# Kernel optimization log

Hardware: AMD Instinct MI355X
Metric: run time of the kernel (lower is better)

Reference implementation:

```python
import jax, jax.numpy as jnp
import numpy as np

def setup_inputs() -> dict:
    key = jax.random.key(0)
    k1, k2, k3, k4, k5 = jax.random.split(key, 5)
    H = 1024
    B, T = 32, 1024
    hidden = jax.random.normal(k1, (1, B, H), dtype=jnp.float32)
    encoder_outputs = jax.random.normal(k2, (B, T, H), dtype=jnp.float32)
    # nn.Linear(2H, H): weight [H, 2H], bias [H]
    bound = 1.0 / np.sqrt(2 * H)
    W = jax.random.uniform(k3, (H, 2 * H), minval=-bound, maxval=bound, dtype=jnp.float32)
    b = jax.random.uniform(k4, (H,), minval=-bound, maxval=bound, dtype=jnp.float32)
    v = jax.random.uniform(k5, (H,), dtype=jnp.float32)  # torch.rand
    return {"hidden": hidden, "encoder_outputs": encoder_outputs, "W": W, "b": b, "v": v}

def reference(hidden, encoder_outputs, W, b, v):
    B = hidden.shape[1]
    H = hidden.shape[2]
    h = jnp.transpose(hidden, (1, 0, 2)).reshape(B, -1)  # [B, H]
    # Split Linear(2H->H): cat([h_rep, enc]) @ W.T == h @ Wh.T + enc @ We.T
    Wh, We = W[:, :H], W[:, H:]
    # [B,1,H] + [B,T,H] -> [B,T,H]
    pre = jnp.tanh((h @ Wh.T + b)[:, None, :] + jnp.einsum('bth,gh->btg', encoder_outputs, We))
    energies = jnp.einsum('bth,h->bt', pre, v)  # [B, T]
    return jax.nn.softmax(energies, axis=1)[:, None, :]  # [B, 1, T]
```

## Files before the change

### kernel.cpp

```cpp
#include <hip/hip_runtime.h>
#include <hip/hip_fp16.h>

typedef _Float16 half8   __attribute__((ext_vector_type(8)));
typedef _Float16 half4_t __attribute__((ext_vector_type(4)));
typedef float    f32x4   __attribute__((ext_vector_type(4)));

#define HDIM  1024
#define BATCH 32
#define TLEN  1024
#define M_TOT (BATCH * TLEN)

#define BM 128
#define BN 128
#define BKF 64
#define LDA 40

__global__ void prep_k(const float* __restrict__ W, const float* __restrict__ hidden,
                       const float* __restrict__ bias, _Float16* __restrict__ We16,
                       float* __restrict__ q, float* __restrict__ energ) {
    const int bid = blockIdx.x;
    const int t = threadIdx.x;
    if (bid < 1024) {
        int idx = bid * 256 + t;
        int g  = idx >> 8;
        int k4 = idx & 255;
        float4 f = *reinterpret_cast<const float4*>(W + (size_t)g * 2048 + 1024 + k4 * 4);
        half4_t h;
        h[0] = (_Float16)f.x; h[1] = (_Float16)f.y; h[2] = (_Float16)f.z; h[3] = (_Float16)f.w;
        *reinterpret_cast<half4_t*>(We16 + (size_t)idx * 4) = h;
    } else if (bid < 2048) {
        int g = bid - 1024;
        int wave = t >> 6, lane = t & 63;
        float acc[BATCH];
#pragma unroll
        for (int b = 0; b < BATCH; b++) acc[b] = 0.f;
        const float* wr = W + (size_t)g * 2048;
        for (int h = t; h < HDIM; h += 256) {
            float w = wr[h];
#pragma unroll
            for (int b = 0; b < BATCH; b++) acc[b] = fmaf(w, hidden[b * HDIM + h], acc[b]);
        }
        __shared__ float sm[4 * BATCH];
#pragma unroll
        for (int b = 0; b < BATCH; b++) {
            float s = acc[b];
#pragma unroll
            for (int off = 32; off >= 1; off >>= 1) s += __shfl_xor(s, off);
            if (lane == 0) sm[wave * BATCH + b] = s;
        }
        __syncthreads();
        if (t < BATCH) {
            float s = sm[t] + sm[BATCH + t] + sm[2 * BATCH + t] + sm[3 * BATCH + t];
            q[t * HDIM + g] = s + bias[g];
        }
    } else {
        energ[(bid - 2048) * 256 + t] = 0.f;
    }
}

__global__ void enc_convert_k(const float* __restrict__ enc, _Float16* __restrict__ enc16) {
    size_t i = ((size_t)blockIdx.x * blockDim.x + threadIdx.x) * 8;
    float4 f0 = *reinterpret_cast<const float4*>(enc + i);
    float4 f1 = *reinterpret_cast<const float4*>(enc + i + 4);
    half8 h;
    h[0] = (_Float16)f0.x; h[1] = (_Float16)f0.y; h[2] = (_Float16)f0.z; h[3] = (_Float16)f0.w;
    h[4] = (_Float16)f1.x; h[5] = (_Float16)f1.y; h[6] = (_Float16)f1.z; h[7] = (_Float16)f1.w;
    *reinterpret_cast<half8*>(enc16 + i) = h;
}

__device__ __forceinline__ void async16(const void* g, void* l) {
    __builtin_amdgcn_global_load_lds(
        (const __attribute__((address_space(1))) void*)g,
        (__attribute__((address_space(3))) void*)l, 16, 0, 0);
}

__global__ __launch_bounds__(256)
void attn_gemm_lds_k(const _Float16* __restrict__ enc16,
                     const _Float16* __restrict__ We16,
                     const float* __restrict__ q, const float* __restrict__ v,
                     float* __restrict__ energies) {
    __shared__ _Float16 As[BM * BKF];
    __shared__ _Float16 Bs[BN * BKF];

    const int tid  = threadIdx.x;
    const int id   = blockIdx.x;
    const int xcd  = id & 7;
    const int w    = id >> 3;
    const int m0   = (xcd * 32 + (w >> 3)) * BM;
    const int n0   = (w & 7) * BN;
    const int wave = tid >> 6;
    const int lane = tid & 63;
    const int quad = lane >> 4;
    const int l16  = lane & 15;
    const int wm   = (wave & 1) * 64;
    const int wn   = (wave >> 1) * 64;

    f32x4 acc[4][4];
#pragma unroll
    for (int i = 0; i < 4; i++)
#pragma unroll
        for (int j = 0; j < 4; j++) acc[i][j] = {0.f, 0.f, 0.f, 0.f};

    const int srow = wave * 32 + (lane >> 3);
    const int scol = ((lane & 7) ^ (lane >> 3)) * 8;
    const _Float16* gA = enc16 + (size_t)(m0 + srow) * HDIM + scol;
    const _Float16* gB = We16  + (size_t)(n0 + srow) * HDIM + scol;
    _Float16* lA = As + wave * 2048;
    _Float16* lB = Bs + wave * 2048;
    const size_t istep = (size_t)8 * HDIM;

#pragma unroll
    for (int ii = 0; ii < 4; ii++) {
        async16(gA + ii * istep, lA + ii * 512);
        async16(gB + ii * istep, lB + ii * 512);
    }
    __syncthreads();

    int aoff[2][4], boff[2][4];
#pragma unroll
    for (int s = 0; s < 2; s++)
#pragma unroll
        for (int i = 0; i < 4; i++) {
            int ra = wm + i * 16 + l16;
            int rb = wn + i * 16 + l16;
            aoff[s][i] = ra * BKF + (((s * 4 + quad) ^ (l16 & 7)) * 8);
            boff[s][i] = rb * BKF + (((s * 4 + quad) ^ (l16 & 7)) * 8);
        }

    for (int k0 = 0; k0 < HDIM; k0 += BKF) {
        half8 af[2][4], bf[2][4];
#pragma unroll
        for (int s = 0; s < 2; s++)
#pragma unroll
            for (int i = 0; i < 4; i++) {
                af[s][i] = *reinterpret_cast<const half8*>(&As[aoff[s][i]]);
                bf[s][i] = *reinterpret_cast<const half8*>(&Bs[boff[s][i]]);
            }
        __syncthreads();

        if (k0 + BKF < HDIM) {
            const int kn = k0 + BKF;
#pragma unroll
            for (int ii = 0; ii < 4; ii++) {
                async16(gA + kn + ii * istep, lA + ii * 512);
                async16(gB + kn + ii * istep, lB + ii * 512);
            }
        }

#pragma unroll
        for (int s = 0; s < 2; s++)
#pragma unroll
            for (int mi = 0; mi < 4; mi++)
#pragma unroll
                for (int ni = 0; ni < 4; ni++)
                    acc[mi][ni] = __builtin_amdgcn_mfma_f32_16x16x32_f16(af[s][mi], bf[s][ni], acc[mi][ni], 0, 0, 0);

        __syncthreads();
    }

    const int bidx = m0 >> 10;
    float qv[4], vv[4];
#pragma unroll
    for (int ni = 0; ni < 4; ni++) {
        int g = n0 + wn + ni * 16 + l16;
        qv[ni] = q[bidx * HDIM + g];
        vv[ni] = v[g];
    }
#pragma unroll
    for (int mi = 0; mi < 4; mi++) {
#pragma unroll
        for (int r = 0; r < 4; r++) {
            int row = wm + mi * 16 + quad * 4 + r;
            float s = 0.f;
#pragma unroll
            for (int ni = 0; ni < 4; ni++) {
                float pre = acc[mi][ni][r] + qv[ni];
                float e = __expf(2.f * pre);
                float th = 1.f - 2.f / (e + 1.f);
                s = fmaf(th, vv[ni], s);
            }
            s += __shfl_xor(s, 1);
            s += __shfl_xor(s, 2);
            s += __shfl_xor(s, 4);
            s += __shfl_xor(s, 8);
            if (l16 == 0) atomicAdd(&energies[m0 + row], s);
        }
    }
}

__global__ __launch_bounds__(256, 2)
void attn_gemm_k(const float* __restrict__ enc, const _Float16* __restrict__ We16,
                 const float* __restrict__ q, const float* __restrict__ v,
                 float* __restrict__ energies) {
    __shared__ _Float16 As[BM * LDA];
    __shared__ _Float16 Bs[BN * LDA];

    const int tid  = threadIdx.x;
    const int m0   = blockIdx.x * BM;
    const int n0   = blockIdx.y * BN;
    const int wave = tid >> 6;
    const int lane = tid & 63;
    const int quad = lane >> 4;
    const int l16  = lane & 15;
    const int wm   = (wave & 1) * 64;
    const int wn   = (wave >> 1) * 64;

    const int srow = tid >> 1;
    const int scol = (tid & 1) * 16;

    f32x4 acc[4][4];
#pragma unroll
    for (int i = 0; i < 4; i++)
#pragma unroll
        for (int j = 0; j < 4; j++) acc[i][j] = {0.f, 0.f, 0.f, 0.f};

    const float*    ag = enc  + (size_t)(m0 + srow) * HDIM + scol;
    const _Float16* bg = We16 + (size_t)(n0 + srow) * HDIM + scol;
    _Float16* aw = &As[srow * LDA + scol];
    _Float16* bw = &Bs[srow * LDA + scol];

    for (int k0 = 0; k0 < HDIM; k0 += 32) {
        float4 a0 = *reinterpret_cast<const float4*>(ag + k0 + 0);
        float4 a1 = *reinterpret_cast<const float4*>(ag + k0 + 4);
        float4 a2 = *reinterpret_cast<const float4*>(ag + k0 + 8);
        float4 a3 = *reinterpret_cast<const float4*>(ag + k0 + 12);
        float4 b0 = *reinterpret_cast<const float4*>(bg + k0);
        float4 b1 = *reinterpret_cast<const float4*>(bg + k0 + 8);

        __syncthreads();

        half8 ha0, ha1;
        ha0[0] = (_Float16)a0.x; ha0[1] = (_Float16)a0.y; ha0[2] = (_Float16)a0.z; ha0[3] = (_Float16)a0.w;
        ha0[4] = (_Float16)a1.x; ha0[5] = (_Float16)a1.y; ha0[6] = (_Float16)a1.z; ha0[7] = (_Float16)a1.w;
        ha1[0] = (_Float16)a2.x; ha1[1] = (_Float16)a2.y; ha1[2] = (_Float16)a2.z; ha1[3] = (_Float16)a2.w;
        ha1[4] = (_Float16)a3.x; ha1[5] = (_Float16)a3.y; ha1[6] = (_Float16)a3.z; ha1[7] = (_Float16)a3.w;
        *reinterpret_cast<half8*>(aw)     = ha0;
        *reinterpret_cast<half8*>(aw + 8) = ha1;
        *reinterpret_cast<float4*>(bw)     = b0;
        *reinterpret_cast<float4*>(bw + 8) = b1;

        __syncthreads();

        half8 af[4], bf[4];
#pragma unroll
        for (int i = 0; i < 4; i++) {
            af[i] = *reinterpret_cast<const half8*>(&As[(wm + i * 16 + l16) * LDA + quad * 8]);
            bf[i] = *reinterpret_cast<const half8*>(&Bs[(wn + i * 16 + l16) * LDA + quad * 8]);
        }
#pragma unroll
        for (int mi = 0; mi < 4; mi++)
#pragma unroll
            for (int ni = 0; ni < 4; ni++)
                acc[mi][ni] = __builtin_amdgcn_mfma_f32_16x16x32_f16(af[mi], bf[ni], acc[mi][ni], 0, 0, 0);
    }

    const int bidx = m0 >> 10;
    float qv[4], vv[4];
#pragma unroll
    for (int ni = 0; ni < 4; ni++) {
        int g = n0 + wn + ni * 16 + l16;
        qv[ni] = q[bidx * HDIM + g];
        vv[ni] = v[g];
    }
#pragma unroll
    for (int mi = 0; mi < 4; mi++) {
#pragma unroll
        for (int r = 0; r < 4; r++) {
            int row = wm + mi * 16 + quad * 4 + r;
            float s = 0.f;
#pragma unroll
            for (int ni = 0; ni < 4; ni++) {
                float pre = acc[mi][ni][r] + qv[ni];
                float e = __expf(2.f * pre);
                float th = 1.f - 2.f / (e + 1.f);
                s = fmaf(th, vv[ni], s);
            }
            s += __shfl_xor(s, 1);
            s += __shfl_xor(s, 2);
            s += __shfl_xor(s, 4);
            s += __shfl_xor(s, 8);
            if (l16 == 0) atomicAdd(&energies[m0 + row], s);
        }
    }
}

__global__ void softmax_k(const float* __restrict__ energies, float* __restrict__ out) {
    int b = blockIdx.x;
    int t = threadIdx.x;
    int wave = t >> 6, lane = t & 63;
    __shared__ float smax[4], ssum[4];
    float e[4];
#pragma unroll
    for (int i = 0; i < 4; i++) e[i] = energies[b * TLEN + t + i * 256];
    float m = fmaxf(fmaxf(e[0], e[1]), fmaxf(e[2], e[3]));
#pragma unroll
    for (int off = 32; off >= 1; off >>= 1) m = fmaxf(m, __shfl_xor(m, off));
    if (lane == 0) smax[wave] = m;
    __syncthreads();
    float M = fmaxf(fmaxf(smax[0], smax[1]), fmaxf(smax[2], smax[3]));
    float x[4]; float s = 0.f;
#pragma unroll
    for (int i = 0; i < 4; i++) { x[i] = __expf(e[i] - M); s += x[i]; }
#pragma unroll
    for (int off = 32; off >= 1; off >>= 1) s += __shfl_xor(s, off);
    if (lane == 0) ssum[wave] = s;
    __syncthreads();
    float S = ssum[0] + ssum[1] + ssum[2] + ssum[3];
    float inv = 1.f / S;
#pragma unroll
    for (int i = 0; i < 4; i++) out[b * TLEN + t + i * 256] = x[i] * inv;
}

extern "C" void kernel_launch(void* const* d_in, const int* in_sizes, int n_in,
                              void* d_out, int out_size, void* d_ws, size_t ws_size,
                              hipStream_t stream) {
    const float* hidden = (const float*)d_in[0];
    const float* enc    = (const float*)d_in[1];
    const float* W      = (const float*)d_in[2];
    const float* bias   = (const float*)d_in[3];
    const float* v      = (const float*)d_in[4];
    float* out = (float*)d_out;

    char* ws = (char*)d_ws;
    float*    q     = (float*)ws;
    float*    energ = (float*)(ws + 131072);
    _Float16* We16  = (_Float16*)(ws + 262144);
    _Float16* enc16 = (_Float16*)(ws + 262144 + 2097152);
    const size_t need_fast = 262144 + 2097152 + (size_t)M_TOT * HDIM * 2;

    prep_k<<<dim3(2176), 256, 0, stream>>>(W, hidden, bias, We16, q, energ);
    if (ws_size >= need_fast) {
        enc_convert_k<<<dim3((size_t)M_TOT * HDIM / 8 / 256), 256, 0, stream>>>(enc, enc16);
        attn_gemm_lds_k<<<dim3(2048), 256, 0, stream>>>(enc16, We16, q, v, energ);
    } else {
        attn_gemm_k<<<dim3(256, 8), 256, 0, stream>>>(enc, We16, q, v, energ);
    }
    softmax_k<<<dim3(BATCH), 256, 0, stream>>>(energ, out);
}
```

Measured before the change: 309.5 us.

## Replace LDS GEMM with 256x256-tile 8-wave double-buffered ping-pong kernel

Swaps the 128x128 single-buffer fp16 GEMM for a 256x256-tile, 512-thread kernel. It double-buffers LDS with direct global-to-LDS loads and interleaves staged fragment reads, MFMA sub-blocks and barriers with setprio hints. The goal is more reuse per loaded byte and hiding global load latency behind MFMA work. In exchange it uses 128KB of LDS per block and many more accumulator registers, and it relies on hand-tuned waitcnt counts for correctness.

```diff
diff --git a/kernel.cpp b/kernel.cpp
--- a/kernel.cpp
+++ b/kernel.cpp
@@ -12,7 +12,6 @@
 
 #define BM 128
 #define BN 128
-#define BKF 64
 #define LDA 40
 
 __global__ void prep_k(const float* __restrict__ W, const float* __restrict__ hidden,
@@ -74,20 +73,169 @@
         (__attribute__((address_space(3))) void*)l, 16, 0, 0);
 }
 
-__global__ __launch_bounds__(256)
-void attn_gemm_lds_k(const _Float16* __restrict__ enc16,
-                     const _Float16* __restrict__ We16,
-                     const float* __restrict__ q, const float* __restrict__ v,
-                     float* __restrict__ energies) {
-    __shared__ _Float16 As[BM * BKF];
-    __shared__ _Float16 Bs[BN * BKF];
+#define NIT 8
+
+__global__ __launch_bounds__(512, 2)
+void attn_gemm8_k(const _Float16* __restrict__ enc16,
+                  const _Float16* __restrict__ We16,
+                  const float* __restrict__ q, const float* __restrict__ v,
+                  float* __restrict__ energies) {
+    __shared__ _Float16 lds[65536];
 
     const int tid  = threadIdx.x;
     const int id   = blockIdx.x;
     const int xcd  = id & 7;
     const int w    = id >> 3;
-    const int m0   = (xcd * 32 + (w >> 3)) * BM;
-    const int n0   = (w & 7) * BN;
+    const int m0   = (xcd * 16 + (w >> 2)) * 256;
+    const int n0   = (w & 3) * 256;
+
+    const int wave = tid >> 6;
+    const int lane = tid & 63;
+    const int quad = lane >> 4;
+    const int l16  = lane & 15;
+    const int wm   = wave >> 2;
+    const int wn   = wave & 3;
+    const int hb   = wn >> 1;
+
+    const int rA = tid >> 3;
+    const int sc = ((tid & 7) ^ (rA & 7)) * 8;
+    const _Float16* gA = enc16 + (size_t)(m0 + rA) * HDIM + sc;
+    const _Float16* gB = We16  + (size_t)(n0 + rA) * HDIM + sc;
+
+    const int cs0 = (quad ^ (l16 & 7)) * 8;
+    const int cs1 = ((4 + quad) ^ (l16 & 7)) * 8;
+    const int arow = wm * 8192 + l16 * 64;
+    const int brow = 16384 + hb * 8192 + ((wn & 1) * 64 + l16) * 64;
+
+    f32x4 acc[8][4];
+#pragma unroll
+    for (int i = 0; i < 8; i++)
+#pragma unroll
+        for (int j = 0; j < 4; j++) acc[i][j] = {0.f, 0.f, 0.f, 0.f};
+
+    half8 aLo[4][2], aHi[4][2], bLo[2][2], bHi[2][2];
+
+#define STAGE_A(buf, ha, kt) do { \
+    _Float16* d_ = &lds[(buf)*32768 + (ha)*8192 + tid*8]; \
+    const _Float16* s_ = gA + (size_t)(ha)*131072 + (kt)*64; \
+    async16(s_, d_); async16(s_ + 65536, d_ + 4096); } while(0)
+
+#define STAGE_B(buf, hbt, kt) do { \
+    _Float16* d_ = &lds[(buf)*32768 + 16384 + (hbt)*8192 + tid*8]; \
+    const _Float16* s_ = gB + (size_t)(hbt)*131072 + (kt)*64; \
+    async16(s_, d_); async16(s_ + 65536, d_ + 4096); } while(0)
+
+#define RD_ALO(bb) { _Pragma("unroll") for (int mi_ = 0; mi_ < 4; mi_++) { \
+    aLo[mi_][0] = *reinterpret_cast<const half8*>(&lds[(bb)+arow+mi_*1024+cs0]); \
+    aLo[mi_][1] = *reinterpret_cast<const half8*>(&lds[(bb)+arow+mi_*1024+cs1]); } }
+#define RD_AHI(bb) { _Pragma("unroll") for (int mi_ = 0; mi_ < 4; mi_++) { \
+    aHi[mi_][0] = *reinterpret_cast<const half8*>(&lds[(bb)+arow+(mi_+4)*1024+cs0]); \
+    aHi[mi_][1] = *reinterpret_cast<const half8*>(&lds[(bb)+arow+(mi_+4)*1024+cs1]); } }
+#define RD_BLO(bb) { _Pragma("unroll") for (int ni_ = 0; ni_ < 2; ni_++) { \
+    bLo[ni_][0] = *reinterpret_cast<const half8*>(&lds[(bb)+brow+ni_*1024+cs0]); \
+    bLo[ni_][1] = *reinterpret_cast<const half8*>(&lds[(bb)+brow+ni_*1024+cs1]); } }
+#define RD_BHI(bb) { _Pragma("unroll") for (int ni_ = 0; ni_ < 2; ni_++) { \
+    bHi[ni_][0] = *reinterpret_cast<const half8*>(&lds[(bb)+brow+(ni_+2)*1024+cs0]); \
+    bHi[ni_][1] = *reinterpret_cast<const half8*>(&lds[(bb)+brow+(ni_+2)*1024+cs1]); } }
+
+#define MFMA16(AF, BF, MO, NO) { _Pragma("unroll") for (int ks_ = 0; ks_ < 2; ks_++) \
+    _Pragma("unroll") for (int mi_ = 0; mi_ < 4; mi_++) \
+    _Pragma("unroll") for (int ni_ = 0; ni_ < 2; ni_++) \
+      acc[mi_+MO][ni_+NO] = __builtin_amdgcn_mfma_f32_16x16x32_f16( \
+          AF[mi_][ks_], BF[ni_][ks_], acc[mi_+MO][ni_+NO], 0, 0, 0); }
+
+#define BAR1 { __builtin_amdgcn_s_barrier(); \
+    asm volatile("s_waitcnt lgkmcnt(0)" ::: "memory"); \
+    __builtin_amdgcn_sched_barrier(0); \
+    __builtin_amdgcn_s_setprio(1); }
+#define BAR2 { __builtin_amdgcn_s_setprio(0); \
+    __builtin_amdgcn_s_barrier(); \
+    __builtin_amdgcn_sched_barrier(0); }
+#define BAR2V(n) { __builtin_amdgcn_s_setprio(0); \
+    asm volatile("s_waitcnt vmcnt(" #n ")" ::: "memory"); \
+    __builtin_amdgcn_s_barrier(); \
+    __builtin_amdgcn_sched_barrier(0); }
+
+    STAGE_A(0, 0, 0); STAGE_A(0, 1, 0); STAGE_B(0, 0, 0); STAGE_B(0, 1, 0);
+    STAGE_B(1, 0, 1); STAGE_B(1, 1, 1);
+    asm volatile("s_waitcnt vmcnt(4)" ::: "memory");
+    __builtin_amdgcn_s_barrier();
+    __builtin_amdgcn_sched_barrier(0);
+
+    for (int i = 0; i < NIT; i++) {
+        const int kt1 = 2 * i + 1, kt2 = 2 * i + 2, kt3 = 2 * i + 3;
+        const bool more = (i < NIT - 1);
+        RD_ALO(0); RD_BLO(0);            STAGE_A(1, 0, kt1);
+        BAR1; MFMA16(aLo, bLo, 0, 0); BAR2;
+        RD_BHI(0);                       STAGE_A(1, 1, kt1);
+        BAR1; MFMA16(aLo, bHi, 0, 2); BAR2;
+        RD_AHI(0);                       if (more) STAGE_B(0, 0, kt2);
+        BAR1; MFMA16(aHi, bHi, 4, 2); BAR2;
+                                         if (more) STAGE_B(0, 1, kt2);
+        BAR1; MFMA16(aHi, bLo, 4, 0);
+        if (more) { BAR2V(4); } else { BAR2V(0); }
+        RD_ALO(32768); RD_BLO(32768);    if (more) STAGE_A(0, 0, kt2);
+        BAR1; MFMA16(aLo, bLo, 0, 0); BAR2;
+        RD_BHI(32768);                   if (more) STAGE_A(0, 1, kt2);
+        BAR1; MFMA16(aLo, bHi, 0, 2); BAR2;
+        RD_AHI(32768);                   if (more) STAGE_B(1, 0, kt3);
+        BAR1; MFMA16(aHi, bHi, 4, 2); BAR2;
+                                         if (more) STAGE_B(1, 1, kt3);
+        BAR1; MFMA16(aHi, bLo, 4, 0);
+        if (more) { BAR2V(4); } else { BAR2; }
+    }
+
+    const int bidx = m0 >> 10;
+    const int gb = n0 + wn * 64;
+    float qv[4], vv[4];
+#pragma unroll
+    for (int ni = 0; ni < 4; ni++) {
+        int g = gb + ni * 16 + l16;
+        qv[ni] = q[bidx * HDIM + g];
+        vv[ni] = v[g];
+    }
+#pragma unroll
+    for (int mi = 0; mi < 8; mi++) {
+#pragma unroll
+        for (int r = 0; r < 4; r++) {
+            int row = m0 + wm * 128 + mi * 16 + quad * 4 + r;
+            float s = 0.f;
+#pragma unroll
+            for (int ni = 0; ni < 4; ni++) {
+                float pre = acc[mi][ni][r] + qv[ni];
+                float e = __expf(2.f * pre);
+                float th = 1.f - 2.f / (e + 1.f);
+                s = fmaf(th, vv[ni], s);
+            }
+            s += __shfl_xor(s, 1);
+            s += __shfl_xor(s, 2);
+            s += __shfl_xor(s, 4);
+            s += __shfl_xor(s, 8);
+            if (l16 == 0) atomicAdd(&energies[row], s);
+        }
+    }
+#undef STAGE_A
+#undef STAGE_B
+#undef RD_ALO
+#undef RD_AHI
+#undef RD_BLO
+#undef RD_BHI
+#undef MFMA16
+#undef BAR1
+#undef BAR2
+#undef BAR2V
+}
+
+__global__ __launch_bounds__(256, 2)
+void attn_gemm_k(const float* __restrict__ enc, const _Float16* __restrict__ We16,
+                 const float* __restrict__ q, const float* __restrict__ v,
+                 float* __restrict__ energies) {
+    __shared__ _Float16 As[BM * LDA];
+    __shared__ _Float16 Bs[BN * LDA];
+
+    const int tid  = threadIdx.x;
+    const int m0   = blockIdx.x * BM;
+    const int n0   = blockIdx.y * BN;
     const int wave = tid >> 6;
     const int lane = tid & 63;
     const int quad = lane >> 4;
@@ -95,67 +243,53 @@
     const int wm   = (wave & 1) * 64;
     const int wn   = (wave >> 1) * 64;
 
+    const int srow = tid >> 1;
+    const int scol = (tid & 1) * 16;
+
     f32x4 acc[4][4];
 #pragma unroll
     for (int i = 0; i < 4; i++)
 #pragma unroll
         for (int j = 0; j < 4; j++) acc[i][j] = {0.f, 0.f, 0.f, 0.f};
 
-    const int srow = wave * 32 + (lane >> 3);
-    const int scol = ((lane & 7) ^ (lane >> 3)) * 8;
-    const _Float16* gA = enc16 + (size_t)(m0 + srow) * HDIM + scol;
-    const _Float16* gB = We16  + (size_t)(n0 + srow) * HDIM + scol;
-    _Float16* lA = As + wave * 2048;
-    _Float16* lB = Bs + wave * 2048;
-    const size_t istep = (size_t)8 * HDIM;
-
-#pragma unroll
-    for (int ii = 0; ii < 4; ii++) {
-        async16(gA + ii * istep, lA + ii * 512);
-        async16(gB + ii * istep, lB + ii * 512);
-    }
-    __syncthreads();
-
-    int aoff[2][4], boff[2][4];
-#pragma unroll
-    for (int s = 0; s < 2; s++)
+    const float*    ag = enc  + (size_t)(m0 + srow) * HDIM + scol;
+    const _Float16* bg = We16 + (size_t)(n0 + srow) * HDIM + scol;
+    _Float16* aw = &As[srow * LDA + scol];
+    _Float16* bw = &Bs[srow * LDA + scol];
+
+    for (int k0 = 0; k0 < HDIM; k0 += 32) {
+        float4 a0 = *reinterpret_cast<const float4*>(ag + k0 + 0);
+        float4 a1 = *reinterpret_cast<const float4*>(ag + k0 + 4);
+        float4 a2 = *reinterpret_cast<const float4*>(ag + k0 + 8);
+        float4 a3 = *reinterpret_cast<const float4*>(ag + k0 + 12);
+        float4 b0 = *reinterpret_cast<const float4*>(bg + k0);
+        float4 b1 = *reinterpret_cast<const float4*>(bg + k0 + 8);
+
+        __syncthreads();
+
+        half8 ha0, ha1;
+        ha0[0] = (_Float16)a0.x; ha0[1] = (_Float16)a0.y; ha0[2] = (_Float16)a0.z; ha0[3] = (_Float16)a0.w;
+        ha0[4] = (_Float16)a1.x; ha0[5] = (_Float16)a1.y; ha0[6] = (_Float16)a1.z; ha0[7] = (_Float16)a1.w;
+        ha1[0] = (_Float16)a2.x; ha1[1] = (_Float16)a2.y; ha1[2] = (_Float16)a2.z; ha1[3] = (_Float16)a2.w;
+        ha1[4] = (_Float16)a3.x; ha1[5] = (_Float16)a3.y; ha1[6] = (_Float16)a3.z; ha1[7] = (_Float16)a3.w;
+        *reinterpret_cast<half8*>(aw)     = ha0;
+        *reinterpret_cast<half8*>(aw + 8) = ha1;
+        *reinterpret_cast<float4*>(bw)     = b0;
+        *reinterpret_cast<float4*>(bw + 8) = b1;
+
+        __syncthreads();
+
+        half8 af[4], bf[4];
 #pragma unroll
         for (int i = 0; i < 4; i++) {
-            int ra = wm + i * 16 + l16;
-            int rb = wn + i * 16 + l16;
-            aoff[s][i] = ra * BKF + (((s * 4 + quad) ^ (l16 & 7)) * 8);
-            boff[s][i] = rb * BKF + (((s * 4 + quad) ^ (l16 & 7)) * 8);
-        }
-
-    for (int k0 = 0; k0 < HDIM; k0 += BKF) {
-        half8 af[2][4], bf[2][4];
-#pragma unroll
-        for (int s = 0; s < 2; s++)
-#pragma unroll
-            for (int i = 0; i < 4; i++) {
-                af[s][i] = *reinterpret_cast<const half8*>(&As[aoff[s][i]]);
-                bf[s][i] = *reinterpret_cast<const half8*>(&Bs[boff[s][i]]);
-            }
-        __syncthreads();
-
-        if (k0 + BKF < HDIM) {
-            const int kn = k0 + BKF;
-#pragma unroll
-            for (int ii = 0; ii < 4; ii++) {
-                async16(gA + kn + ii * istep, lA + ii * 512);
-                async16(gB + kn + ii * istep, lB + ii * 512);
-            }
-        }
-
-#pragma unroll
-        for (int s = 0; s < 2; s++)
-#pragma unroll
-            for (int mi = 0; mi < 4; mi++)
-#pragma unroll
-                for (int ni = 0; ni < 4; ni++)
-                    acc[mi][ni] = __builtin_amdgcn_mfma_f32_16x16x32_f16(af[s][mi], bf[s][ni], acc[mi][ni], 0, 0, 0);
-
-        __syncthreads();
+            af[i] = *reinterpret_cast<const half8*>(&As[(wm + i * 16 + l16) * LDA + quad * 8]);
+            bf[i] = *reinterpret_cast<const half8*>(&Bs[(wn + i * 16 + l16) * LDA + quad * 8]);
+        }
+#pragma unroll
+        for (int mi = 0; mi < 4; mi++)
+#pragma unroll
+            for (int ni = 0; ni < 4; ni++)
+                acc[mi][ni] = __builtin_amdgcn_mfma_f32_16x16x32_f16(af[mi], bf[ni], acc[mi][ni], 0, 0, 0);
     }
 
     const int bidx = m0 >> 10;
@@ -188,102 +322,6 @@
     }
 }
 
-__global__ __launch_bounds__(256, 2)
-void attn_gemm_k(const float* __restrict__ enc, const _Float16* __restrict__ We16,
-                 const float* __restrict__ q, const float* __restrict__ v,
-                 float* __restrict__ energies) {
-    __shared__ _Float16 As[BM * LDA];
-    __shared__ _Float16 Bs[BN * LDA];
-
-    const int tid  = threadIdx.x;
-    const int m0   = blockIdx.x * BM;
-    const int n0   = blockIdx.y * BN;
-    const int wave = tid >> 6;
-    const int lane = tid & 63;
-    const int quad = lane >> 4;
-    const int l16  = lane & 15;
-    const int wm   = (wave & 1) * 64;
-    const int wn   = (wave >> 1) * 64;
-
-    const int srow = tid >> 1;
-    const int scol = (tid & 1) * 16;
-
-    f32x4 acc[4][4];
-#pragma unroll
-    for (int i = 0; i < 4; i++)
-#pragma unroll
-        for (int j = 0; j < 4; j++) acc[i][j] = {0.f, 0.f, 0.f, 0.f};
-
-    const float*    ag = enc  + (size_t)(m0 + srow) * HDIM + scol;
-    const _Float16* bg = We16 + (size_t)(n0 + srow) * HDIM + scol;
-    _Float16* aw = &As[srow * LDA + scol];
-    _Float16* bw = &Bs[srow * LDA + scol];
-
-    for (int k0 = 0; k0 < HDIM; k0 += 32) {
-        float4 a0 = *reinterpret_cast<const float4*>(ag + k0 + 0);
-        float4 a1 = *reinterpret_cast<const float4*>(ag + k0 + 4);
-        float4 a2 = *reinterpret_cast<const float4*>(ag + k0 + 8);
-        float4 a3 = *reinterpret_cast<const float4*>(ag + k0 + 12);
-        float4 b0 = *reinterpret_cast<const float4*>(bg + k0);
-        float4 b1 = *reinterpret_cast<const float4*>(bg + k0 + 8);
-
-        __syncthreads();
-
-        half8 ha0, ha1;
-        ha0[0] = (_Float16)a0.x; ha0[1] = (_Float16)a0.y; ha0[2] = (_Float16)a0.z; ha0[3] = (_Float16)a0.w;
-        ha0[4] = (_Float16)a1.x; ha0[5] = (_Float16)a1.y; ha0[6] = (_Float16)a1.z; ha0[7] = (_Float16)a1.w;
-        ha1[0] = (_Float16)a2.x; ha1[1] = (_Float16)a2.y; ha1[2] = (_Float16)a2.z; ha1[3] = (_Float16)a2.w;
-        ha1[4] = (_Float16)a3.x; ha1[5] = (_Float16)a3.y; ha1[6] = (_Float16)a3.z; ha1[7] = (_Float16)a3.w;
-        *reinterpret_cast<half8*>(aw)     = ha0;
-        *reinterpret_cast<half8*>(aw + 8) = ha1;
-        *reinterpret_cast<float4*>(bw)     = b0;
-        *reinterpret_cast<float4*>(bw + 8) = b1;
-
-        __syncthreads();
-
-        half8 af[4], bf[4];
-#pragma unroll
-        for (int i = 0; i < 4; i++) {
-            af[i] = *reinterpret_cast<const half8*>(&As[(wm + i * 16 + l16) * LDA + quad * 8]);
-            bf[i] = *reinterpret_cast<const half8*>(&Bs[(wn + i * 16 + l16) * LDA + quad * 8]);
-        }
-#pragma unroll
-        for (int mi = 0; mi < 4; mi++)
-#pragma unroll
-            for (int ni = 0; ni < 4; ni++)
-                acc[mi][ni] = __builtin_amdgcn_mfma_f32_16x16x32_f16(af[mi], bf[ni], acc[mi][ni], 0, 0, 0);
-    }
-
-    const int bidx = m0 >> 10;
-    float qv[4], vv[4];
-#pragma unroll
-    for (int ni = 0; ni < 4; ni++) {
-        int g = n0 + wn + ni * 16 + l16;
-        qv[ni] = q[bidx * HDIM + g];
-        vv[ni] = v[g];
-    }
-#pragma unroll
-    for (int mi = 0; mi < 4; mi++) {
-#pragma unroll
-        for (int r = 0; r < 4; r++) {
-            int row = wm + mi * 16 + quad * 4 + r;
-            float s = 0.f;
-#pragma unroll
-            for (int ni = 0; ni < 4; ni++) {
-                float pre = acc[mi][ni][r] + qv[ni];
-                float e = __expf(2.f * pre);
-                float th = 1.f - 2.f / (e + 1.f);
-                s = fmaf(th, vv[ni], s);
-            }
-            s += __shfl_xor(s, 1);
-            s += __shfl_xor(s, 2);
-            s += __shfl_xor(s, 4);
-            s += __shfl_xor(s, 8);
-            if (l16 == 0) atomicAdd(&energies[m0 + row], s);
-        }
-    }
-}
-
 __global__ void softmax_k(const float* __restrict__ energies, float* __restrict__ out) {
     int b = blockIdx.x;
     int t = threadIdx.x;
@@ -331,7 +369,7 @@
     prep_k<<<dim3(2176), 256, 0, stream>>>(W, hidden, bias, We16, q, energ);
     if (ws_size >= need_fast) {
         enc_convert_k<<<dim3((size_t)M_TOT * HDIM / 8 / 256), 256, 0, stream>>>(enc, enc16);
-        attn_gemm_lds_k<<<dim3(2048), 256, 0, stream>>>(enc16, We16, q, v, energ);
+        attn_gemm8_k<<<dim3(512), 512, 0, stream>>>(enc16, We16, q, v, energ);
     } else {
         attn_gemm_k<<<dim3(256, 8), 256, 0, stream>>>(enc, We16, q, v, energ);
     }
```

New measurement: 306.0 us. Within noise of the previous version (-1.1%).

## Fuse fp32-to-fp16 encoder conversion into the attention GEMM A-tile load

Applied to the files above, without the earlier changes.

Removes the standalone enc_convert kernel and its fp16 workspace copy. The GEMM now loads fp32 encoder rows into registers one K-step ahead, converts them to fp16 and writes them into swizzled LDS after the MFMAs. The B operand keeps using async global-to-LDS loads. This saves a full write and re-read of the converted tensor, in exchange for fp32 A traffic that each of the 8 N-blocks re-reads, more register pressure, and manual waitcnt and barrier scheduling.

```diff
diff --git a/kernel.cpp b/kernel.cpp
--- a/kernel.cpp
+++ b/kernel.cpp
@@ -58,16 +58,6 @@
     }
 }
 
-__global__ void enc_convert_k(const float* __restrict__ enc, _Float16* __restrict__ enc16) {
-    size_t i = ((size_t)blockIdx.x * blockDim.x + threadIdx.x) * 8;
-    float4 f0 = *reinterpret_cast<const float4*>(enc + i);
-    float4 f1 = *reinterpret_cast<const float4*>(enc + i + 4);
-    half8 h;
-    h[0] = (_Float16)f0.x; h[1] = (_Float16)f0.y; h[2] = (_Float16)f0.z; h[3] = (_Float16)f0.w;
-    h[4] = (_Float16)f1.x; h[5] = (_Float16)f1.y; h[6] = (_Float16)f1.z; h[7] = (_Float16)f1.w;
-    *reinterpret_cast<half8*>(enc16 + i) = h;
-}
-
 __device__ __forceinline__ void async16(const void* g, void* l) {
     __builtin_amdgcn_global_load_lds(
         (const __attribute__((address_space(1))) void*)g,
@@ -75,10 +65,10 @@
 }
 
 __global__ __launch_bounds__(256)
-void attn_gemm_lds_k(const _Float16* __restrict__ enc16,
-                     const _Float16* __restrict__ We16,
-                     const float* __restrict__ q, const float* __restrict__ v,
-                     float* __restrict__ energies) {
+void attn_gemm_f32a_k(const float* __restrict__ enc,
+                      const _Float16* __restrict__ We16,
+                      const float* __restrict__ q, const float* __restrict__ v,
+                      float* __restrict__ energies) {
     __shared__ _Float16 As[BM * BKF];
     __shared__ _Float16 Bs[BN * BKF];
 
@@ -103,18 +93,29 @@
 
     const int srow = wave * 32 + (lane >> 3);
     const int scol = ((lane & 7) ^ (lane >> 3)) * 8;
-    const _Float16* gA = enc16 + (size_t)(m0 + srow) * HDIM + scol;
-    const _Float16* gB = We16  + (size_t)(n0 + srow) * HDIM + scol;
-    _Float16* lA = As + wave * 2048;
+    const _Float16* gB = We16 + (size_t)(n0 + srow) * HDIM + scol;
     _Float16* lB = Bs + wave * 2048;
     const size_t istep = (size_t)8 * HDIM;
 
-#pragma unroll
-    for (int ii = 0; ii < 4; ii++) {
-        async16(gA + ii * istep, lA + ii * 512);
-        async16(gB + ii * istep, lB + ii * 512);
-    }
-    __syncthreads();
+    const int arow_s = tid >> 3;
+    const int ac     = tid & 7;
+    const float* gA = enc + (size_t)(m0 + arow_s) * HDIM + ac * 8;
+    _Float16* aw = As + arow_s * BKF + ((ac ^ (arow_s & 7)) * 8);
+
+    float4 fa[4][2];
+
+#define ISSUE_A(kk) { _Pragma("unroll") for (int p_ = 0; p_ < 4; p_++) { \
+    const float* s_ = gA + (size_t)(p_ * 32) * HDIM + (kk); \
+    fa[p_][0] = *reinterpret_cast<const float4*>(s_); \
+    fa[p_][1] = *reinterpret_cast<const float4*>(s_ + 4); } }
+
+#define CVT_WRITE_A() { _Pragma("unroll") for (int p_ = 0; p_ < 4; p_++) { \
+    half8 h_; \
+    h_[0] = (_Float16)fa[p_][0].x; h_[1] = (_Float16)fa[p_][0].y; \
+    h_[2] = (_Float16)fa[p_][0].z; h_[3] = (_Float16)fa[p_][0].w; \
+    h_[4] = (_Float16)fa[p_][1].x; h_[5] = (_Float16)fa[p_][1].y; \
+    h_[6] = (_Float16)fa[p_][1].z; h_[7] = (_Float16)fa[p_][1].w; \
+    *reinterpret_cast<half8*>(aw + p_ * 32 * BKF) = h_; } }
 
     int aoff[2][4], boff[2][4];
 #pragma unroll
@@ -127,7 +128,18 @@
             boff[s][i] = rb * BKF + (((s * 4 + quad) ^ (l16 & 7)) * 8);
         }
 
+    ISSUE_A(0);
+#pragma unroll
+    for (int ii = 0; ii < 4; ii++) async16(gB + ii * istep, lB + ii * 512);
+    CVT_WRITE_A();
+    asm volatile("s_waitcnt vmcnt(0) lgkmcnt(0)" ::: "memory");
+    __builtin_amdgcn_s_barrier();
+    __builtin_amdgcn_sched_barrier(0);
+
     for (int k0 = 0; k0 < HDIM; k0 += BKF) {
+        const bool more = (k0 + BKF) < HDIM;
+        if (more) ISSUE_A(k0 + BKF);
+
         half8 af[2][4], bf[2][4];
 #pragma unroll
         for (int s = 0; s < 2; s++)
@@ -136,15 +148,15 @@
                 af[s][i] = *reinterpret_cast<const half8*>(&As[aoff[s][i]]);
                 bf[s][i] = *reinterpret_cast<const half8*>(&Bs[boff[s][i]]);
             }
-        __syncthreads();
-
-        if (k0 + BKF < HDIM) {
+        asm volatile("s_waitcnt lgkmcnt(0)" ::: "memory");
+        __builtin_amdgcn_sched_barrier(0);
+        __builtin_amdgcn_s_barrier();
+        __builtin_amdgcn_sched_barrier(0);
+
+        if (more) {
             const int kn = k0 + BKF;
 #pragma unroll
-            for (int ii = 0; ii < 4; ii++) {
-                async16(gA + kn + ii * istep, lA + ii * 512);
-                async16(gB + kn + ii * istep, lB + ii * 512);
-            }
+            for (int ii = 0; ii < 4; ii++) async16(gB + kn + ii * istep, lB + ii * 512);
         }
 
 #pragma unroll
@@ -155,8 +167,17 @@
                 for (int ni = 0; ni < 4; ni++)
                     acc[mi][ni] = __builtin_amdgcn_mfma_f32_16x16x32_f16(af[s][mi], bf[s][ni], acc[mi][ni], 0, 0, 0);
 
-        __syncthreads();
-    }
+        __builtin_amdgcn_sched_barrier(0);
+
+        if (more) {
+            CVT_WRITE_A();
+            asm volatile("s_waitcnt vmcnt(0) lgkmcnt(0)" ::: "memory");
+            __builtin_amdgcn_s_barrier();
+            __builtin_amdgcn_sched_barrier(0);
+        }
+    }
+#undef ISSUE_A
+#undef CVT_WRITE_A
 
     const int bidx = m0 >> 10;
     float qv[4], vv[4];
@@ -325,13 +346,11 @@
     float*    q     = (float*)ws;
     float*    energ = (float*)(ws + 131072);
     _Float16* We16  = (_Float16*)(ws + 262144);
-    _Float16* enc16 = (_Float16*)(ws + 262144 + 2097152);
-    const size_t need_fast = 262144 + 2097152 + (size_t)M_TOT * HDIM * 2;
+    const size_t need_fast = 262144 + 2097152;
 
     prep_k<<<dim3(2176), 256, 0, stream>>>(W, hidden, bias, We16, q, energ);
     if (ws_size >= need_fast) {
-        enc_convert_k<<<dim3((size_t)M_TOT * HDIM / 8 / 256), 256, 0, stream>>>(enc, enc16);
-        attn_gemm_lds_k<<<dim3(2048), 256, 0, stream>>>(enc16, We16, q, v, energ);
+        attn_gemm_f32a_k<<<dim3(2048), 256, 0, stream>>>(enc, We16, q, v, energ);
     } else {
         attn_gemm_k<<<dim3(256, 8), 256, 0, stream>>>(enc, We16, q, v, energ);
     }
```

After: 465.2 us. +50.3%, slower.

## Fuse fp32-to-fp16 encoder conversion into GEMM LDS load path

Applied to the files above, without the earlier changes.

Removes the separate kernel that converted the whole encoder tensor to fp16 in workspace. The GEMM now async-copies fp32 encoder tiles straight into LDS with an XOR swizzle and converts them to half8 fragments when reading LDS for MFMA. This drops a full read of the fp32 tensor plus a write and re-read of the fp16 copy. In exchange the A tile doubles in LDS size, which may lower occupancy, each A tile is fetched from L2/HBM at twice the bytes, and the inner loop gains conversion VALU work.

```diff
diff --git a/kernel.cpp b/kernel.cpp
--- a/kernel.cpp
+++ b/kernel.cpp
@@ -58,16 +58,6 @@
     }
 }
 
-__global__ void enc_convert_k(const float* __restrict__ enc, _Float16* __restrict__ enc16) {
-    size_t i = ((size_t)blockIdx.x * blockDim.x + threadIdx.x) * 8;
-    float4 f0 = *reinterpret_cast<const float4*>(enc + i);
-    float4 f1 = *reinterpret_cast<const float4*>(enc + i + 4);
-    half8 h;
-    h[0] = (_Float16)f0.x; h[1] = (_Float16)f0.y; h[2] = (_Float16)f0.z; h[3] = (_Float16)f0.w;
-    h[4] = (_Float16)f1.x; h[5] = (_Float16)f1.y; h[6] = (_Float16)f1.z; h[7] = (_Float16)f1.w;
-    *reinterpret_cast<half8*>(enc16 + i) = h;
-}
-
 __device__ __forceinline__ void async16(const void* g, void* l) {
     __builtin_amdgcn_global_load_lds(
         (const __attribute__((address_space(1))) void*)g,
@@ -75,11 +65,11 @@
 }
 
 __global__ __launch_bounds__(256)
-void attn_gemm_lds_k(const _Float16* __restrict__ enc16,
-                     const _Float16* __restrict__ We16,
-                     const float* __restrict__ q, const float* __restrict__ v,
-                     float* __restrict__ energies) {
-    __shared__ _Float16 As[BM * BKF];
+void attn_gemm_f32d_k(const float* __restrict__ enc,
+                      const _Float16* __restrict__ We16,
+                      const float* __restrict__ q, const float* __restrict__ v,
+                      float* __restrict__ energies) {
+    __shared__ float    Asf[BM * BKF];
     __shared__ _Float16 Bs[BN * BKF];
 
     const int tid  = threadIdx.x;
@@ -101,31 +91,43 @@
 #pragma unroll
         for (int j = 0; j < 4; j++) acc[i][j] = {0.f, 0.f, 0.f, 0.f};
 
-    const int srow = wave * 32 + (lane >> 3);
-    const int scol = ((lane & 7) ^ (lane >> 3)) * 8;
-    const _Float16* gA = enc16 + (size_t)(m0 + srow) * HDIM + scol;
-    const _Float16* gB = We16  + (size_t)(n0 + srow) * HDIM + scol;
-    _Float16* lA = As + wave * 2048;
+    const int srowB = wave * 32 + (lane >> 3);
+    const int scolB = ((lane & 7) ^ (lane >> 3)) * 8;
+    const _Float16* gB = We16 + (size_t)(n0 + srowB) * HDIM + scolB;
     _Float16* lB = Bs + wave * 2048;
-    const size_t istep = (size_t)8 * HDIM;
-
-#pragma unroll
-    for (int ii = 0; ii < 4; ii++) {
-        async16(gA + ii * istep, lA + ii * 512);
-        async16(gB + ii * istep, lB + ii * 512);
-    }
+    const size_t istepB = (size_t)8 * HDIM;
+
+    const int lr = lane >> 4;
+    const int cA = lane & 15;
+    const float* pA[4];
+#pragma unroll
+    for (int j = 0; j < 4; j++)
+        pA[j] = enc + (size_t)(m0 + wave * 32 + lr) * HDIM + ((cA ^ (j * 4 + lr)) * 4);
+    float* lA = Asf + wave * 2048;
+
+    int boff[2][4];
+#pragma unroll
+    for (int s = 0; s < 2; s++)
+#pragma unroll
+        for (int i = 0; i < 4; i++)
+            boff[s][i] = (wn + i * 16 + l16) * BKF + (((s * 4 + quad) ^ (l16 & 7)) * 8);
+    int arow[4];
+#pragma unroll
+    for (int i = 0; i < 4; i++) arow[i] = (wm + i * 16 + l16) * BKF;
+    int acol[2][2];
+#pragma unroll
+    for (int s = 0; s < 2; s++)
+#pragma unroll
+        for (int j = 0; j < 2; j++)
+            acol[s][j] = ((((s * 4 + quad) * 2 + j) ^ l16) * 4);
+
+#pragma unroll
+    for (int ii = 0; ii < 8; ii++)
+        async16(pA[ii & 3] + (size_t)(ii * 4) * HDIM, lA + ii * 256);
+#pragma unroll
+    for (int ii = 0; ii < 4; ii++)
+        async16(gB + ii * istepB, lB + ii * 512);
     __syncthreads();
-
-    int aoff[2][4], boff[2][4];
-#pragma unroll
-    for (int s = 0; s < 2; s++)
-#pragma unroll
-        for (int i = 0; i < 4; i++) {
-            int ra = wm + i * 16 + l16;
-            int rb = wn + i * 16 + l16;
-            aoff[s][i] = ra * BKF + (((s * 4 + quad) ^ (l16 & 7)) * 8);
-            boff[s][i] = rb * BKF + (((s * 4 + quad) ^ (l16 & 7)) * 8);
-        }
 
     for (int k0 = 0; k0 < HDIM; k0 += BKF) {
         half8 af[2][4], bf[2][4];
@@ -133,7 +135,14 @@
         for (int s = 0; s < 2; s++)
 #pragma unroll
             for (int i = 0; i < 4; i++) {
-                af[s][i] = *reinterpret_cast<const half8*>(&As[aoff[s][i]]);
+                f32x4 a0 = *reinterpret_cast<const f32x4*>(&Asf[arow[i] + acol[s][0]]);
+                f32x4 a1 = *reinterpret_cast<const f32x4*>(&Asf[arow[i] + acol[s][1]]);
+                half8 h;
+                h[0] = (_Float16)a0[0]; h[1] = (_Float16)a0[1];
+                h[2] = (_Float16)a0[2]; h[3] = (_Float16)a0[3];
+                h[4] = (_Float16)a1[0]; h[5] = (_Float16)a1[1];
+                h[6] = (_Float16)a1[2]; h[7] = (_Float16)a1[3];
+                af[s][i] = h;
                 bf[s][i] = *reinterpret_cast<const half8*>(&Bs[boff[s][i]]);
             }
         __syncthreads();
@@ -141,10 +150,11 @@
         if (k0 + BKF < HDIM) {
             const int kn = k0 + BKF;
 #pragma unroll
-            for (int ii = 0; ii < 4; ii++) {
-                async16(gA + kn + ii * istep, lA + ii * 512);
-                async16(gB + kn + ii * istep, lB + ii * 512);
-            }
+            for (int ii = 0; ii < 8; ii++)
+                async16(pA[ii & 3] + (size_t)(ii * 4) * HDIM + kn, lA + ii * 256);
+#pragma unroll
+            for (int ii = 0; ii < 4; ii++)
+                async16(gB + kn + ii * istepB, lB + ii * 512);
         }
 
 #pragma unroll
@@ -325,13 +335,11 @@
     float*    q     = (float*)ws;
     float*    energ = (float*)(ws + 131072);
     _Float16* We16  = (_Float16*)(ws + 262144);
-    _Float16* enc16 = (_Float16*)(ws + 262144 + 2097152);
-    const size_t need_fast = 262144 + 2097152 + (size_t)M_TOT * HDIM * 2;
+    const size_t need = 262144 + 2097152;
 
     prep_k<<<dim3(2176), 256, 0, stream>>>(W, hidden, bias, We16, q, energ);
-    if (ws_size >= need_fast) {
-        enc_convert_k<<<dim3((size_t)M_TOT * HDIM / 8 / 256), 256, 0, stream>>>(enc, enc16);
-        attn_gemm_lds_k<<<dim3(2048), 256, 0, stream>>>(enc16, We16, q, v, energ);
+    if (ws_size >= need) {
+        attn_gemm_f32d_k<<<dim3(2048), 256, 0, stream>>>(enc, We16, q, v, energ);
     } else {
         attn_gemm_k<<<dim3(256, 8), 256, 0, stream>>>(enc, We16, q, v, energ);
     }
```

Result: slower. 333.1 us (+7.6%).
